# Performance work log

Hardware: AMD Instinct MI355X
Metric: run time of the kernel (lower is better)

## Reference

```python
import jax, jax.numpy as jnp
import numpy as np

B, T, D = 2, 2048, 2048
HQ, HKV, HD = 16, 8, 128
GROUP = HQ // HKV
EPS = 1e-6


def rms_norm(x, scale):
    # qwen3-compatible: compute in fp32
    xf = x.astype(jnp.float32)
    var = jnp.mean(xf * xf, axis=-1, keepdims=True)
    return (xf * jax.lax.rsqrt(var + EPS) * scale).astype(x.dtype)


def apply_rope(x, cos, sin):
    # x: [B,H,T,d]; cos,sin: [T,d]
    d2 = x.shape[-1] // 2
    x1, x2 = x[..., :d2], x[..., d2:]
    rot = jnp.concatenate([-x2, x1], axis=-1)
    return (x * cos[None, None] + rot * sin[None, None]).astype(x.dtype)


def setup_inputs() -> dict:
    key = jax.random.key(0)
    ks = jax.random.split(key, 8)
    x = jax.random.normal(ks[0], (B, T, D), dtype=jnp.float32)
    # causal mask: True where attention is disallowed (j > i)
    mask = jnp.triu(jnp.ones((T, T), dtype=jnp.bool_), k=1)
    # RoPE tables
    inv_freq = 1.0 / (10000.0 ** (np.arange(0, HD, 2, dtype=np.float32) / HD))
    pos = np.arange(T, dtype=np.float32)
    ang = np.outer(pos, inv_freq)  # [T, HD/2]
    ang = np.concatenate([ang, ang], axis=-1)  # [T, HD]
    cos = jnp.asarray(np.cos(ang), dtype=jnp.float32)
    sin = jnp.asarray(np.sin(ang), dtype=jnp.float32)
    s = 0.02
    Wq = jax.random.normal(ks[1], (HQ * HD, D), dtype=jnp.float32) * s
    Wk = jax.random.normal(ks[2], (HKV * HD, D), dtype=jnp.float32) * s
    Wv = jax.random.normal(ks[3], (HKV * HD, D), dtype=jnp.float32) * s
    Wo = jax.random.normal(ks[4], (D, HQ * HD), dtype=jnp.float32) * s
    q_scale = jnp.ones((HD,), dtype=jnp.float32)
    k_scale = jnp.ones((HD,), dtype=jnp.float32)
    return {"x": x, "mask": mask, "cos": cos, "sin": sin,
            "Wq": Wq, "Wk": Wk, "Wv": Wv, "Wo": Wo,
            "q_scale": q_scale, "k_scale": k_scale}


def reference(x, mask, cos, sin, Wq, Wk, Wv, Wo, q_scale, k_scale):
    Bc, Tc, _ = x.shape
    Q = jnp.einsum('btd,ed->bte', x, Wq).reshape(Bc, Tc, HQ, HD).transpose(0, 2, 1, 3)
    K = jnp.einsum('btd,ed->bte', x, Wk).reshape(Bc, Tc, HKV, HD).transpose(0, 2, 1, 3)
    V = jnp.einsum('btd,ed->bte', x, Wv).reshape(Bc, Tc, HKV, HD).transpose(0, 2, 1, 3)
    Q = rms_norm(Q, q_scale)
    K = rms_norm(K, k_scale)
    Q = apply_rope(Q, cos, sin)
    K = apply_rope(K, cos, sin)
    K = jnp.repeat(K, GROUP, axis=1)  # [B,HQ,T,d]
    V = jnp.repeat(V, GROUP, axis=1)
    S = jnp.einsum('bhqd,bhkd->bhqk', Q, K) / jnp.sqrt(jnp.float32(HD))
    S = jnp.where(mask[None, None], -jnp.inf, S)
    P = jax.nn.softmax(S, axis=-1)
    ctx = jnp.einsum('bhqk,bhkd->bhqd', P, V).transpose(0, 2, 1, 3).reshape(Bc, Tc, HQ * HD)
    return jnp.einsum('bte,de->btd', ctx, Wo)
```

## Files before the change

kernel.cpp:

```cpp
#include <hip/hip_runtime.h>
#include <cstdint>
#include <cstddef>

#define B_ 2
#define T_ 2048
#define D_ 2048
#define HQ_ 16
#define HKV_ 8
#define HD_ 128

typedef __attribute__((ext_vector_type(8))) short short8;
typedef __attribute__((ext_vector_type(8))) unsigned short ushort8;
typedef __attribute__((ext_vector_type(4))) float f32x4;
typedef __attribute__((ext_vector_type(2))) unsigned short ushort2v;
typedef __attribute__((ext_vector_type(4))) unsigned short ushort4v;
typedef __attribute__((ext_vector_type(2))) float float2v;
typedef __attribute__((ext_vector_type(4))) float float4v;

__device__ __forceinline__ unsigned short f2bf(float f) {
  unsigned int u = __builtin_bit_cast(unsigned int, f);
  u += 0x7fffu + ((u >> 16) & 1u);
  return (unsigned short)(u >> 16);
}
__device__ __forceinline__ float bf2f(unsigned short h) {
  unsigned int u = ((unsigned int)h) << 16;
  return __builtin_bit_cast(float, u);
}

#if defined(__has_builtin)
#if __has_builtin(__builtin_amdgcn_global_load_lds)
#define HAS_GLL 1
#endif
#endif
#ifndef HAS_GLL
#define HAS_GLL 0
#endif

__device__ __forceinline__ void gll16(const void* g, void* l) {
#if HAS_GLL
  __builtin_amdgcn_global_load_lds((const __attribute__((address_space(1))) void*)g,
                                   (__attribute__((address_space(3))) void*)l, 16, 0, 0);
#else
  *(ushort8*)((char*)l + (threadIdx.x & 63) * 16) = *(const ushort8*)g;
#endif
}

__global__ __launch_bounds__(256) void cast_all(const float* __restrict__ x,
                                                const float* __restrict__ wq,
                                                const float* __restrict__ wk,
                                                const float* __restrict__ wv,
                                                const float* __restrict__ wo,
                                                unsigned short* __restrict__ xb,
                                                unsigned short* __restrict__ wqkv,
                                                unsigned short* __restrict__ wob) {
  int i = (blockIdx.x * 256 + threadIdx.x) * 4;
  if (i >= 20971520) return;
  const float* s;
  unsigned short* d;
  int soff, doff;
  if (i < 8388608)       { s = x;  soff = i;            d = xb;   doff = i; }
  else if (i < 12582912) { s = wq; soff = i - 8388608;  d = wqkv; doff = i - 8388608; }
  else if (i < 14680064) { s = wk; soff = i - 12582912; d = wqkv; doff = i - 8388608; }
  else if (i < 16777216) { s = wv; soff = i - 14680064; d = wqkv; doff = i - 8388608; }
  else                   { s = wo; soff = i - 16777216; d = wob;  doff = i - 16777216; }
  float4v v = *(const float4v*)(s + soff);
  ushort4v o; o.x = f2bf(v.x); o.y = f2bf(v.y); o.z = f2bf(v.z); o.w = f2bf(v.w);
  *(ushort4v*)(d + doff) = o;
}

#define PH_SYNC { __builtin_amdgcn_s_barrier(); \
                  asm volatile("s_waitcnt lgkmcnt(0)" ::: "memory"); \
                  __builtin_amdgcn_sched_barrier(0); \
                  __builtin_amdgcn_s_setprio(1); }
#define PH_END  { __builtin_amdgcn_s_setprio(0); \
                  __builtin_amdgcn_s_barrier(); \
                  __builtin_amdgcn_sched_barrier(0); }

#define LDA(BUF, QM) { \
  _Pragma("unroll") for (int ii = 0; ii < BM/64; ii++) { \
    _Pragma("unroll") for (int ks = 0; ks < 2; ks++) \
      a[ii][ks] = *(const short8*)&Abuf[BUF][((QM)*(BM/2) + wm*(BM/4) + ii*16 + c)*64 + (((ks*4+g)^cs)*8)]; } }

#define LDB(BUF, QN, BB) { \
  _Pragma("unroll") for (int jj = 0; jj < 2; jj++) { \
    _Pragma("unroll") for (int ks = 0; ks < 2; ks++) \
      BB[jj][ks] = *(const short8*)&Bbuf[BUF][((QN)*128 + wn*32 + jj*16 + c)*64 + (((ks*4+g)^cs)*8)]; } }

#define MM(QM, QN, BB) { \
  _Pragma("unroll") for (int ii = 0; ii < BM/64; ii++) { \
    _Pragma("unroll") for (int jj = 0; jj < 2; jj++) { \
      f32x4 t_ = __builtin_amdgcn_mfma_f32_16x16x32_bf16(a[ii][0], BB[jj][0], acc[(QM)*(BM/64)+ii][(QN)*2+jj], 0, 0, 0); \
      acc[(QM)*(BM/64)+ii][(QN)*2+jj] = __builtin_amdgcn_mfma_f32_16x16x32_bf16(a[ii][1], BB[jj][1], t_, 0, 0, 0); } } }

template<int BM, int M, int N, int K, bool BF16_OUT>
__global__ __launch_bounds__(512, 2) void gemm8(const unsigned short* __restrict__ A,
                                                const unsigned short* __restrict__ W,
                                                void* __restrict__ Cout) {
  __shared__ __align__(16) unsigned short Abuf[2][BM * 64];
  __shared__ __align__(16) unsigned short Bbuf[2][256 * 64];
  const int tid = threadIdx.x;
  const int lane = tid & 63;
  const int wv = tid >> 6;
  const int g = lane >> 4;
  const int c = lane & 15;
  const int cs = c & 7;
  const int wm = wv >> 2;
  const int wn = wv & 3;

  constexpr int SH_Q = (BM == 256) ? 7 : 6;
  constexpr int SH_W = SH_Q - 1;

  constexpr int NT = N / 256;
  constexpr int NWG = (M / BM) * NT;
  constexpr int CHUNK = NWG / 8;
  const int bid = blockIdx.x;
  const int swz = (bid & 7) * CHUNK + (bid >> 3);
  const int m0 = (swz / NT) * BM;
  const int n0 = (swz % NT) * 256;

  const int prl = wv * 8 + (lane >> 3);
  const int scl = lane & 7;
#define STA(BUF, P0, KO) { \
    int pr_ = (P0) + prl; \
    int lr_ = ((pr_ >> SH_W) & 1) * (BM/2) + ((pr_ >> SH_Q) & 1) * (BM/4) + (pr_ & (BM/4 - 1)); \
    int lc_ = (scl ^ (pr_ & 7)) * 8; \
    gll16(&A[(size_t)(m0 + lr_) * K + (KO) + lc_], &Abuf[BUF][(P0) * 64 + wv * 512]); }
#define STB(BUF, P0, KO) { \
    int pr_ = (P0) + prl; \
    int lr_ = ((pr_ >> 5) & 3) * 64 + ((pr_ >> 7) & 1) * 32 + (pr_ & 31); \
    int lc_ = (scl ^ (pr_ & 7)) * 8; \
    gll16(&W[(size_t)(n0 + lr_) * K + (KO) + lc_], &Bbuf[BUF][(P0) * 64 + wv * 512]); }

#define STAGE_PH2(BUF, KO) { if constexpr (BM == 256) { STA(BUF, 0, KO); STA(BUF, 64, KO); } \
                             else { STA(BUF, 0, KO); } \
                             STB(BUF, 0, KO); STB(BUF, 64, KO); }
#define STAGE_PH3(BUF, KO) { STB(BUF, 128, KO); STB(BUF, 192, KO); }
#define STAGE_PH4(BUF, KO) { if constexpr (BM == 256) { STA(BUF, 128, KO); STA(BUF, 192, KO); } \
                             else { STA(BUF, 64, KO); } }
#define VMW { if constexpr (BM == 256) { asm volatile("s_waitcnt vmcnt(8)" ::: "memory"); } \
              else { asm volatile("s_waitcnt vmcnt(6)" ::: "memory"); } }

  short8 a[BM/64][2], b0[2][2], b1[2][2];
  f32x4 acc[BM/32][4];
#pragma unroll
  for (int i = 0; i < BM/32; i++)
#pragma unroll
    for (int j = 0; j < 4; j++) acc[i][j] = (f32x4)0.0f;

  STAGE_PH2(0, 0); STAGE_PH3(0, 0); STAGE_PH4(0, 0);
  STAGE_PH2(1, 64); STAGE_PH3(1, 64); STAGE_PH4(1, 64);
  VMW;
  __builtin_amdgcn_s_barrier();

  constexpr int NITER = K / 128;
  for (int it = 0; it < NITER - 1; ++it) {
    const int k2 = it * 128 + 128;
    const int k3 = k2 + 64;
    LDA(0, 0); LDB(0, 0, b0);
    PH_SYNC; MM(0, 0, b0); PH_END;
    LDB(0, 1, b1);
    STAGE_PH2(0, k2);
    PH_SYNC; MM(0, 1, b1); PH_END;
    LDA(0, 1);
    STAGE_PH3(0, k2);
    PH_SYNC; MM(1, 1, b1); PH_END;
    STAGE_PH4(0, k2);
    VMW;
    PH_SYNC; MM(1, 0, b0); PH_END;
    LDA(1, 0); LDB(1, 0, b0);
    PH_SYNC; MM(0, 0, b0); PH_END;
    LDB(1, 1, b1);
    STAGE_PH2(1, k3);
    PH_SYNC; MM(0, 1, b1); PH_END;
    LDA(1, 1);
    STAGE_PH3(1, k3);
    PH_SYNC; MM(1, 1, b1); PH_END;
    STAGE_PH4(1, k3);
    VMW;
    PH_SYNC; MM(1, 0, b0); PH_END;
  }
  LDA(0, 0); LDB(0, 0, b0); PH_SYNC; MM(0, 0, b0); PH_END;
  LDB(0, 1, b1);            PH_SYNC; MM(0, 1, b1); PH_END;
  LDA(0, 1);                PH_SYNC; MM(1, 1, b1); PH_END;
  asm volatile("s_waitcnt vmcnt(0)" ::: "memory");
  PH_SYNC; MM(1, 0, b0); PH_END;
  LDA(1, 0); LDB(1, 0, b0); PH_SYNC; MM(0, 0, b0); PH_END;
  LDB(1, 1, b1);            PH_SYNC; MM(0, 1, b1); PH_END;
  LDA(1, 1);                PH_SYNC; MM(1, 1, b1); PH_END;
  PH_SYNC; MM(1, 0, b0); PH_END;

#pragma unroll
  for (int I = 0; I < BM/32; I++)
#pragma unroll
    for (int J = 0; J < 4; J++)
#pragma unroll
      for (int r = 0; r < 4; r++) {
        int row = m0 + wm * (BM/2) + I * 16 + g * 4 + r;
        int col = n0 + wn * 64 + J * 16 + c;
        if (BF16_OUT)
          ((unsigned short*)Cout)[(size_t)row * N + col] = f2bf(acc[I][J][r]);
        else
          ((float*)Cout)[(size_t)row * N + col] = acc[I][J][r];
      }
#undef STA
#undef STB
#undef STAGE_PH2
#undef STAGE_PH3
#undef STAGE_PH4
#undef VMW
}

__global__ __launch_bounds__(256) void qk_norm_rope(const unsigned short* __restrict__ qkv,
                                                    const float* __restrict__ cosT,
                                                    const float* __restrict__ sinT,
                                                    const float* __restrict__ q_scale,
                                                    const float* __restrict__ k_scale,
                                                    unsigned short* __restrict__ Qb,
                                                    unsigned short* __restrict__ Kb) {
  const int tid = threadIdx.x;
  const int lane = tid & 63;
  const int wv = tid >> 6;
  const int row = blockIdx.x;
  const int b = row >> 11;
  const int t = row & 2047;
  const int d0 = lane * 2;

  const float2v cs = *(const float2v*)&cosT[t * 128 + d0];
  const float2v sn = *(const float2v*)&sinT[t * 128 + d0];
  const float2v qsc = *(const float2v*)&q_scale[d0];
  const float2v ksc = *(const float2v*)&k_scale[d0];
  const float sgn = (lane < 32) ? -1.0f : 1.0f;
  const unsigned short* base = qkv + (size_t)row * 4096;

#pragma unroll
  for (int s6 = 0; s6 < 6; s6++) {
    const int slot = wv * 6 + s6;
    const bool isQ = slot < 16;
    const unsigned short* src = base + (isQ ? slot * 128 : 2048 + (slot - 16) * 128);
    ushort2v u = *(const ushort2v*)&src[d0];
    float x0 = bf2f(u.x), x1 = bf2f(u.y);
    float ss = x0 * x0 + x1 * x1;
    ss += __shfl_xor(ss, 1);  ss += __shfl_xor(ss, 2);  ss += __shfl_xor(ss, 4);
    ss += __shfl_xor(ss, 8);  ss += __shfl_xor(ss, 16); ss += __shfl_xor(ss, 32);
    float rinv = rsqrtf(ss * (1.0f / 128.0f) + 1e-6f);
    float2v scv = isQ ? qsc : ksc;
    float xn0 = x0 * rinv * scv.x;
    float xn1 = x1 * rinv * scv.y;
    float o0 = __shfl_xor(xn0, 32);
    float o1 = __shfl_xor(xn1, 32);
    float r0v = xn0 * cs.x + sgn * o0 * sn.x;
    float r1v = xn1 * cs.y + sgn * o1 * sn.y;
    ushort2v out; out.x = f2bf(r0v); out.y = f2bf(r1v);
    unsigned short* dst;
    if (isQ) dst = Qb + ((size_t)(b * HQ_ + slot) * T_ + t) * HD_;
    else     dst = Kb + ((size_t)(b * HKV_ + (slot - 16)) * T_ + t) * HD_;
    *(ushort2v*)&dst[d0] = out;
  }
}

__global__ __launch_bounds__(256) void v_transpose(const unsigned short* __restrict__ qkv,
                                                   unsigned short* __restrict__ Vt) {
  __shared__ unsigned short lds[128 * 65];
  const int tid = threadIdx.x;
  const int blk = blockIdx.x;
  const int tblk = blk & 31;
  const int kv = (blk >> 5) & 7;
  const int b = blk >> 8;
  const int t0 = tblk * 64;
  const int r = tid >> 2;
  const int seg = tid & 3;
  const unsigned short* src = qkv + (size_t)(b * T_ + t0 + r) * 4096 + 3072 + kv * 128;
  for (int i = 0; i < 4; i++) {
    int cc = seg * 32 + i * 8;
    ushort8 v = *(const ushort8*)&src[cc];
    for (int q = 0; q < 8; q++) lds[(cc + q) * 65 + r] = v[q];
  }
  __syncthreads();
  const int cI = tid >> 1;
  const int rs = (tid & 1) * 32;
  unsigned short* dst = Vt + ((size_t)(b * HKV_ + kv) * HD_ + cI) * T_ + t0 + rs;
  const unsigned short* srow = &lds[cI * 65 + rs];
  for (int j = 0; j < 32; j += 4) {
    ushort4v v; v.x = srow[j]; v.y = srow[j + 1]; v.z = srow[j + 2]; v.w = srow[j + 3];
    *(ushort4v*)&dst[j] = v;
  }
}

__global__ __launch_bounds__(256) void attn(const unsigned short* __restrict__ Qb,
                                            const unsigned short* __restrict__ Kb,
                                            const unsigned short* __restrict__ Vt,
                                            unsigned short* __restrict__ ctxb) {
  __shared__ __align__(16) unsigned short Ks[2][64 * 128];
  __shared__ __align__(16) unsigned short Vs[2][128 * 64];
  __shared__ __align__(16) unsigned short Ps[4][16 * 72];
  const int tid = threadIdx.x;
  const int lane = tid & 63;
  const int wv = tid >> 6;
  const int g = lane >> 4;
  const int c = lane & 15;

  const int blk = blockIdx.x;
  const int kv = blk & 7;
  const int idx = blk >> 3;
  const int p = idx >> 2;
  const int b = (idx >> 1) & 1;
  const int h = kv * 2 + (idx & 1);

  const unsigned short* Kh = Kb + (size_t)(b * HKV_ + kv) * T_ * HD_;
  const unsigned short* Vh = Vt + (size_t)(b * HKV_ + kv) * HD_ * T_;
  const float scale = 0.08838834764831845f;

#define STAGE_KV(BF, KT) { \
  _Pragma("unroll") for (int i_ = 0; i_ < 4; i_++) { \
    const int ch_ = wv * 256 + i_ * 64 + lane; \
    const int rK_ = ch_ >> 4, cK_ = ch_ & 15; \
    gll16(Kh + (size_t)((KT) * 64 + rK_) * HD_ + (cK_ ^ (rK_ & 7)) * 8, \
          Ks[BF] + (size_t)(wv * 256 + i_ * 64) * 8); \
    const int rV_ = ch_ >> 3, cV_ = ch_ & 7; \
    gll16(Vh + (size_t)rV_ * T_ + (KT) * 64 + (cV_ ^ (rV_ & 7)) * 8, \
          Vs[BF] + (size_t)(wv * 256 + i_ * 64) * 8); } }

  for (int ph = 0; ph < 2; ph++) {
    const int qb = ph ? (31 - p) : p;
    const int nkt = qb + 1;
    const unsigned short* Qh = Qb + ((size_t)(b * HQ_ + h) * T_ + qb * 64 + wv * 16) * HD_;

    short8 aq[4];
#pragma unroll
    for (int dk = 0; dk < 4; dk++) aq[dk] = *(const short8*)&Qh[c * HD_ + dk * 32 + g * 8];

    f32x4 acc[8];
#pragma unroll
    for (int dc = 0; dc < 8; dc++) acc[dc] = (f32x4)0.0f;
    float lp[4] = {0.0f, 0.0f, 0.0f, 0.0f};

    STAGE_KV(0, 0);
    __syncthreads();

    for (int kt = 0; kt < nkt; kt++) {
      const int cur = kt & 1;
      if (kt + 1 < nkt) { STAGE_KV(cur ^ 1, kt + 1); }
      __builtin_amdgcn_sched_barrier(0);

      f32x4 s[4];
#pragma unroll
      for (int kf = 0; kf < 4; kf++) s[kf] = (f32x4)0.0f;
      __builtin_amdgcn_s_setprio(1);
#pragma unroll
      for (int dk = 0; dk < 4; dk++) {
#pragma unroll
        for (int kf = 0; kf < 4; kf++) {
          short8 bk = *(const short8*)&Ks[cur][(kf * 16 + c) * 128 + ((dk * 4 + g) ^ (c & 7)) * 8];
          s[kf] = __builtin_amdgcn_mfma_f32_16x16x32_bf16(aq[dk], bk, s[kf], 0, 0, 0);
        }
      }
      __builtin_amdgcn_s_setprio(0);

      const bool diag = (kt == nkt - 1);
#pragma unroll
      for (int kf = 0; kf < 4; kf++) {
#pragma unroll
        for (int r = 0; r < 4; r++) {
          float pv = __expf(s[kf][r] * scale);
          if (diag) {
            int key = kt * 64 + kf * 16 + c;
            int rowq = qb * 64 + wv * 16 + g * 4 + r;
            if (key > rowq) pv = 0.0f;
          }
          lp[r] += pv;
          Ps[wv][(g * 4 + r) * 72 + kf * 16 + c] = f2bf(pv);
        }
      }

      short8 ap[2];
      ap[0] = *(const short8*)&Ps[wv][c * 72 + g * 8];
      ap[1] = *(const short8*)&Ps[wv][c * 72 + 32 + g * 8];
      __builtin_amdgcn_s_setprio(1);
#pragma unroll
      for (int dc = 0; dc < 8; dc++) {
#pragma unroll
        for (int kf2 = 0; kf2 < 2; kf2++) {
          short8 bv = *(const short8*)&Vs[cur][(dc * 16 + c) * 64 + ((kf2 * 4 + g) ^ (c & 7)) * 8];
          acc[dc] = __builtin_amdgcn_mfma_f32_16x16x32_bf16(ap[kf2], bv, acc[dc], 0, 0, 0);
        }
      }
      __builtin_amdgcn_s_setprio(0);

      __syncthreads();
    }

#pragma unroll
    for (int r = 0; r < 4; r++) {
      float l = lp[r];
      l += __shfl_xor(l, 1); l += __shfl_xor(l, 2);
      l += __shfl_xor(l, 4); l += __shfl_xor(l, 8);
      float inv = 1.0f / l;
      int row = b * T_ + qb * 64 + wv * 16 + g * 4 + r;
#pragma unroll
      for (int dc = 0; dc < 8; dc++)
        ctxb[(size_t)row * (HQ_ * HD_) + h * HD_ + dc * 16 + c] = f2bf(acc[dc][r] * inv);
    }
  }
#undef STAGE_KV
}

extern "C" void kernel_launch(void* const* d_in, const int* in_sizes, int n_in,
                              void* d_out, int out_size, void* d_ws, size_t ws_size,
                              hipStream_t stream) {
  const float* x = (const float*)d_in[0];
  const float* cosT = (const float*)d_in[2];
  const float* sinT = (const float*)d_in[3];
  const float* Wq = (const float*)d_in[4];
  const float* Wk = (const float*)d_in[5];
  const float* Wv = (const float*)d_in[6];
  const float* Wo = (const float*)d_in[7];
  const float* q_scale = (const float*)d_in[8];
  const float* k_scale = (const float*)d_in[9];

  char* ws = (char*)d_ws;
  unsigned short* qkv  = (unsigned short*)(ws + 0);
  unsigned short* ctxb = qkv;
  unsigned short* xb   = (unsigned short*)(ws + 33554432);
  unsigned short* wqkv = (unsigned short*)(ws + 50331648);
  unsigned short* wob  = (unsigned short*)(ws + 67108864);
  unsigned short* Qb   = (unsigned short*)(ws + 75497472);
  unsigned short* Kb   = (unsigned short*)(ws + 92274688);
  unsigned short* Vt   = (unsigned short*)(ws + 100663296);

  cast_all<<<20480, 256, 0, stream>>>(x, Wq, Wk, Wv, Wo, xb, wqkv, wob);
  gemm8<256, 4096, 4096, 2048, true><<<256, 512, 0, stream>>>(xb, wqkv, qkv);
  qk_norm_rope<<<4096, 256, 0, stream>>>(qkv, cosT, sinT, q_scale, k_scale, Qb, Kb);
  v_transpose<<<512, 256, 0, stream>>>(qkv, Vt);
  attn<<<512, 256, 0, stream>>>(Qb, Kb, Vt, ctxb);
  gemm8<128, 4096, 2048, 2048, false><<<256, 512, 0, stream>>>(ctxb, wob, d_out);
}
```

Measured before the change: 328.8 us.

## Process both GQA query heads per block sharing staged K/V tiles

Each attention block now handles the two query heads that share one KV head, so each staged K/V tile feeds twice the MFMA work. The old scheme of pairing two causal query tiles per block is replaced by one query tile per block with zigzag ordering, and launch bounds now request two blocks per CU. This cuts global/LDS K/V staging per unit of work, at the cost of doubled accumulator registers, added scheduling barriers, and a change in load balance across blocks.

New measurement: 345.1 us. +5.0%, slower.

```diff
diff --git a/kernel.cpp b/kernel.cpp
--- a/kernel.cpp
+++ b/kernel.cpp
@@ -286,10 +286,10 @@
   }
 }
 
-__global__ __launch_bounds__(256) void attn(const unsigned short* __restrict__ Qb,
-                                            const unsigned short* __restrict__ Kb,
-                                            const unsigned short* __restrict__ Vt,
-                                            unsigned short* __restrict__ ctxb) {
+__global__ __launch_bounds__(256, 2) void attn(const unsigned short* __restrict__ Qb,
+                                               const unsigned short* __restrict__ Kb,
+                                               const unsigned short* __restrict__ Vt,
+                                               unsigned short* __restrict__ ctxb) {
   __shared__ __align__(16) unsigned short Ks[2][64 * 128];
   __shared__ __align__(16) unsigned short Vs[2][128 * 64];
   __shared__ __align__(16) unsigned short Ps[4][16 * 72];
@@ -302,9 +302,10 @@
   const int blk = blockIdx.x;
   const int kv = blk & 7;
   const int idx = blk >> 3;
-  const int p = idx >> 2;
-  const int b = (idx >> 1) & 1;
-  const int h = kv * 2 + (idx & 1);
+  const int b = idx & 1;
+  const int qbi = idx >> 1;
+  const int qb = (qbi < 16) ? qbi : (47 - qbi);
+  const int nkt = qb + 1;
 
   const unsigned short* Kh = Kb + (size_t)(b * HKV_ + kv) * T_ * HD_;
   const unsigned short* Vh = Vt + (size_t)(b * HKV_ + kv) * HD_ * T_;
@@ -320,28 +321,33 @@
     gll16(Vh + (size_t)rV_ * T_ + (KT) * 64 + (cV_ ^ (rV_ & 7)) * 8, \
           Vs[BF] + (size_t)(wv * 256 + i_ * 64) * 8); } }
 
-  for (int ph = 0; ph < 2; ph++) {
-    const int qb = ph ? (31 - p) : p;
-    const int nkt = qb + 1;
-    const unsigned short* Qh = Qb + ((size_t)(b * HQ_ + h) * T_ + qb * 64 + wv * 16) * HD_;
-
-    short8 aq[4];
-#pragma unroll
-    for (int dk = 0; dk < 4; dk++) aq[dk] = *(const short8*)&Qh[c * HD_ + dk * 32 + g * 8];
-
-    f32x4 acc[8];
-#pragma unroll
-    for (int dc = 0; dc < 8; dc++) acc[dc] = (f32x4)0.0f;
-    float lp[4] = {0.0f, 0.0f, 0.0f, 0.0f};
-
-    STAGE_KV(0, 0);
-    __syncthreads();
-
-    for (int kt = 0; kt < nkt; kt++) {
-      const int cur = kt & 1;
-      if (kt + 1 < nkt) { STAGE_KV(cur ^ 1, kt + 1); }
-      __builtin_amdgcn_sched_barrier(0);
-
+  short8 aq[2][4];
+#pragma unroll
+  for (int hh = 0; hh < 2; hh++) {
+    const unsigned short* Qh =
+        Qb + ((size_t)(b * HQ_ + kv * 2 + hh) * T_ + qb * 64 + wv * 16) * HD_;
+#pragma unroll
+    for (int dk = 0; dk < 4; dk++) aq[hh][dk] = *(const short8*)&Qh[c * HD_ + dk * 32 + g * 8];
+  }
+
+  f32x4 acc[2][8];
+#pragma unroll
+  for (int hh = 0; hh < 2; hh++)
+#pragma unroll
+    for (int dc = 0; dc < 8; dc++) acc[hh][dc] = (f32x4)0.0f;
+  float lp[2][4] = {{0.0f, 0.0f, 0.0f, 0.0f}, {0.0f, 0.0f, 0.0f, 0.0f}};
+
+  STAGE_KV(0, 0);
+  __syncthreads();
+
+  for (int kt = 0; kt < nkt; kt++) {
+    const int cur = kt & 1;
+    if (kt + 1 < nkt) { STAGE_KV(cur ^ 1, kt + 1); }
+    __builtin_amdgcn_sched_barrier(0);
+
+    const bool diag = (kt == nkt - 1);
+#pragma unroll
+    for (int hh = 0; hh < 2; hh++) {
       f32x4 s[4];
 #pragma unroll
       for (int kf = 0; kf < 4; kf++) s[kf] = (f32x4)0.0f;
@@ -351,12 +357,11 @@
 #pragma unroll
         for (int kf = 0; kf < 4; kf++) {
           short8 bk = *(const short8*)&Ks[cur][(kf * 16 + c) * 128 + ((dk * 4 + g) ^ (c & 7)) * 8];
-          s[kf] = __builtin_amdgcn_mfma_f32_16x16x32_bf16(aq[dk], bk, s[kf], 0, 0, 0);
+          s[kf] = __builtin_amdgcn_mfma_f32_16x16x32_bf16(aq[hh][dk], bk, s[kf], 0, 0, 0);
         }
       }
       __builtin_amdgcn_s_setprio(0);
 
-      const bool diag = (kt == nkt - 1);
 #pragma unroll
       for (int kf = 0; kf < 4; kf++) {
 #pragma unroll
@@ -367,38 +372,44 @@
             int rowq = qb * 64 + wv * 16 + g * 4 + r;
             if (key > rowq) pv = 0.0f;
           }
-          lp[r] += pv;
+          lp[hh][r] += pv;
           Ps[wv][(g * 4 + r) * 72 + kf * 16 + c] = f2bf(pv);
         }
       }
+      __builtin_amdgcn_sched_barrier(0);
 
       short8 ap[2];
       ap[0] = *(const short8*)&Ps[wv][c * 72 + g * 8];
       ap[1] = *(const short8*)&Ps[wv][c * 72 + 32 + g * 8];
+      __builtin_amdgcn_sched_barrier(0);
       __builtin_amdgcn_s_setprio(1);
 #pragma unroll
       for (int dc = 0; dc < 8; dc++) {
 #pragma unroll
         for (int kf2 = 0; kf2 < 2; kf2++) {
           short8 bv = *(const short8*)&Vs[cur][(dc * 16 + c) * 64 + ((kf2 * 4 + g) ^ (c & 7)) * 8];
-          acc[dc] = __builtin_amdgcn_mfma_f32_16x16x32_bf16(ap[kf2], bv, acc[dc], 0, 0, 0);
+          acc[hh][dc] = __builtin_amdgcn_mfma_f32_16x16x32_bf16(ap[kf2], bv, acc[hh][dc], 0, 0, 0);
         }
       }
       __builtin_amdgcn_s_setprio(0);
-
-      __syncthreads();
     }
 
+    __syncthreads();
+  }
+
+#pragma unroll
+  for (int hh = 0; hh < 2; hh++) {
+    const int h = kv * 2 + hh;
 #pragma unroll
     for (int r = 0; r < 4; r++) {
-      float l = lp[r];
+      float l = lp[hh][r];
       l += __shfl_xor(l, 1); l += __shfl_xor(l, 2);
       l += __shfl_xor(l, 4); l += __shfl_xor(l, 8);
       float inv = 1.0f / l;
       int row = b * T_ + qb * 64 + wv * 16 + g * 4 + r;
 #pragma unroll
       for (int dc = 0; dc < 8; dc++)
-        ctxb[(size_t)row * (HQ_ * HD_) + h * HD_ + dc * 16 + c] = f2bf(acc[dc][r] * inv);
+        ctxb[(size_t)row * (HQ_ * HD_) + h * HD_ + dc * 16 + c] = f2bf(acc[hh][dc][r] * inv);
     }
   }
 #undef STAGE_KV
```
